# Kernel tuning notes

Hardware: AMD Instinct MI355X
Metric: run time of the kernel (lower is better)

The kernel has to match this reference:

```python
import jax, jax.numpy as jnp
import numpy as np

NUM_CLASSES = 20
MIN_CLASS_SIZE = 5000
EPS = 1e-6

B, C, H, W = 2, 64, 384, 384


def setup_inputs() -> dict:
    key = jax.random.key(0)
    k1, k2, k3 = jax.random.split(key, 3)
    hyperspectral_image = jax.random.normal(k1, (B, C, H, W), dtype=jnp.float32)
    methane_pattern = jax.random.normal(k2, (C,), dtype=jnp.float32)
    segmentation_mask = jax.random.randint(k3, (B, H, W), 0, NUM_CLASSES, dtype=jnp.int32)
    return {
        "hyperspectral_image": hyperspectral_image,
        "methane_pattern": methane_pattern,
        "segmentation_mask": segmentation_mask,
    }


def reference(hyperspectral_image, methane_pattern, segmentation_mask):
    b, c, h, w = hyperspectral_image.shape
    n = h * w
    # pixels: (B, N, C); seg: (B, N)
    x = jnp.transpose(hyperspectral_image, (0, 2, 3, 1)).reshape(b, n, c)
    seg = segmentation_mask.reshape(b, n)
    onehot = jax.nn.one_hot(seg, NUM_CLASSES, dtype=x.dtype)  # (B, N, K)

    counts = onehot.sum(axis=1)                                # (B, K)
    safe_counts = jnp.maximum(counts, 1.0)
    sums = jnp.einsum('bnk,bnc->bkc', onehot, x)               # (B, K, C)
    mean = sums / safe_counts[..., None]                       # (B, K, C)

    # Second moment per class: X_k^T X_k, then cov = E[xx^T] - mu mu^T + eps*I
    sxx = jnp.einsum('bnk,bnc,bnd->bkcd', onehot, x, x)        # (B, K, C, C)
    cov = sxx / safe_counts[..., None, None] - jnp.einsum('bkc,bkd->bkcd', mean, mean)
    cov = cov + EPS * jnp.eye(c, dtype=x.dtype)
    inv_cov = jnp.linalg.inv(cov)                              # (B, K, C, C)

    p = methane_pattern
    w_filt = jnp.einsum('bkcd,d->bkc', inv_cov, p)             # Sigma^-1 p, (B, K, C)
    denom = jnp.sqrt(jnp.einsum('c,bkc->bk', p, w_filt))       # (B, K)

    valid = (counts >= MIN_CLASS_SIZE).astype(x.dtype)         # (B, K)

    # Gather per-pixel class stats via one-hot (exact partition)
    mean_px = jnp.einsum('bnk,bkc->bnc', onehot, mean)         # (B, N, C)
    w_px = jnp.einsum('bnk,bkc->bnc', onehot, w_filt)          # (B, N, C)
    denom_px = jnp.einsum('bnk,bk->bn', onehot, denom)         # (B, N)
    valid_px = jnp.einsum('bnk,bk->bn', onehot, valid)         # (B, N)

    score = jnp.sum((x - mean_px) * w_px, axis=-1) / denom_px  # (B, N)
    score = score * valid_px
    return score.reshape(b, h, w)
```

## Files before the change

kernel.cpp:

```cpp
#include <hip/hip_runtime.h>
#include <math.h>

#define NCLS 20
#define CH 64
#define NPIX (384*384)
#define BATCH 2
#define MINSZ 5000
#define EPSV 1e-6f
#define NCHUNK 16
#define NBLK (BATCH*NPIX/256)
#define BLKPERB (NPIX/256)
#define PSTRIDE 4160
#define XSTR 72
#define ROWOFF(c) ((c)*XSTR + ((c)>>3)*8)

typedef __attribute__((ext_vector_type(8))) __bf16 bf16x8;
typedef __attribute__((ext_vector_type(4))) float  f32x4;

static __device__ inline unsigned short f2bf(float f) {
    unsigned u = __builtin_bit_cast(unsigned, f);
    return (unsigned short)((u + 0x7fffu + ((u >> 16) & 1u)) >> 16);
}
static __device__ inline float bf2f(unsigned us) {
    unsigned u = us << 16;
    return __builtin_bit_cast(float, u);
}

__global__ void k_hist(const int* __restrict__ seg, int* __restrict__ hist) {
    __shared__ int h[NCLS];
    int t = threadIdx.x;
    if (t < NCLS) h[t] = 0;
    __syncthreads();
    int k = seg[blockIdx.x * 256 + t];
    atomicAdd(&h[k], 1);
    __syncthreads();
    if (t < NCLS) hist[blockIdx.x * NCLS + t] = h[t];
}

__global__ void __launch_bounds__(256) k_scanall(const int* __restrict__ hist,
        int* __restrict__ counts, int* __restrict__ blockbase, int* __restrict__ offsets) {
    int bk = blockIdx.x;
    int b = bk / NCLS, k = bk % NCLS;
    int t = threadIdx.x;
    __shared__ int sh[BLKPERB];
    __shared__ int part[NCLS][12];
    __shared__ int ctot[NCLS];
    __shared__ int tpA[256], tpB[256];
    __shared__ int soff;

    const int* hb = hist + (size_t)b * BLKPERB * NCLS;
    for (int e = t; e < BLKPERB; e += 256) sh[e] = hb[e * NCLS + k];
    if (t < NCLS * 12) {
        int kk = t / 12, sub = t % 12;
        int s = 0;
        #pragma unroll 8
        for (int e = sub * 48; e < sub * 48 + 48; ++e) s += hb[e * NCLS + kk];
        part[kk][sub] = s;
    }
    __syncthreads();
    if (t < NCLS) {
        int s = 0;
        #pragma unroll
        for (int j = 0; j < 12; ++j) s += part[t][j];
        ctot[t] = s;
    }
    __syncthreads();
    if (t == 0) {
        int off = b * NPIX;
        for (int kk = 0; kk < k; ++kk) off += ctot[kk];
        soff = off;
        offsets[bk] = off;
        counts[bk] = ctot[k];
    }
    int s0 = 0, s1 = 0, s2 = 0;
    if (t < 192) {
        s0 = sh[3*t];
        s1 = s0 + sh[3*t + 1];
        s2 = s1 + sh[3*t + 2];
    }
    int mytot = (t < 192) ? s2 : 0;
    tpA[t] = mytot;
    __syncthreads();
    tpB[t] = tpA[t] + ((t >= 1)   ? tpA[t-1]   : 0); __syncthreads();
    tpA[t] = tpB[t] + ((t >= 2)   ? tpB[t-2]   : 0); __syncthreads();
    tpB[t] = tpA[t] + ((t >= 4)   ? tpA[t-4]   : 0); __syncthreads();
    tpA[t] = tpB[t] + ((t >= 8)   ? tpB[t-8]   : 0); __syncthreads();
    tpB[t] = tpA[t] + ((t >= 16)  ? tpA[t-16]  : 0); __syncthreads();
    tpA[t] = tpB[t] + ((t >= 32)  ? tpB[t-32]  : 0); __syncthreads();
    tpB[t] = tpA[t] + ((t >= 64)  ? tpA[t-64]  : 0); __syncthreads();
    tpA[t] = tpB[t] + ((t >= 128) ? tpB[t-128] : 0); __syncthreads();
    if (t < 192) {
        int excl = soff + tpA[t] - mytot;
        int* bb = blockbase + ((size_t)b * BLKPERB) * NCLS + k;
        bb[(3*t    ) * NCLS] = excl;
        bb[(3*t + 1) * NCLS] = excl + s0;
        bb[(3*t + 2) * NCLS] = excl + s1;
    }
}

__global__ void __launch_bounds__(256) k_scatter(const float* __restrict__ x, const int* __restrict__ seg,
                          const int* __restrict__ blockbase, unsigned short* __restrict__ gathered) {
    __shared__ float tile[256 * 33];
    __shared__ int wcnt[4][NCLS];
    __shared__ int sblk[NCLS];
    __shared__ int drow[256];
    int t = threadIdx.x;
    int blk = blockIdx.x;
    int base = blk * 256;
    int b = base / NPIX;
    int n = (base % NPIX) + t;
    int k = seg[base + t];
    int wave = t >> 6, lane = t & 63;

    int riw = 0;
    for (int cls = 0; cls < NCLS; ++cls) {
        unsigned long long m = __ballot(k == cls);
        if (lane == 0) wcnt[wave][cls] = __popcll(m);
        if (k == cls) riw = __popcll(m & ((1ull << lane) - 1ull));
    }
    __syncthreads();
    if (t < NCLS) {
        int s = 0;
        for (int c = 0; c < t; ++c) s += wcnt[0][c] + wcnt[1][c] + wcnt[2][c] + wcnt[3][c];
        sblk[t] = s;
    }
    __syncthreads();
    int rib = riw;
    for (int w = 0; w < 4; ++w) if (w < wave) rib += wcnt[w][k];
    int slot = sblk[k] + rib;
    drow[slot] = blockbase[blk * NCLS + k] + rib;
    const float* xb = x + (size_t)b * CH * NPIX + n;

    for (int ph = 0; ph < 2; ++ph) {
        __syncthreads();
        #pragma unroll 8
        for (int c = 0; c < 32; ++c)
            tile[slot * 33 + c] = xb[(size_t)(ph * 32 + c) * NPIX];
        __syncthreads();
        #pragma unroll 8
        for (int it = 0; it < 16; ++it) {
            int f = it * 256 + t;
            int r = f >> 4, c2 = f & 15;
            float a = tile[r * 33 + c2 * 2];
            float bq = tile[r * 33 + c2 * 2 + 1];
            unsigned pk = (unsigned)f2bf(a) | ((unsigned)f2bf(bq) << 16);
            *(unsigned*)(gathered + (size_t)drow[r] * CH + ph * 32 + c2 * 2) = pk;
        }
    }
}

__global__ void __launch_bounds__(256) k_gemm(const unsigned short* __restrict__ gathered,
        const int* __restrict__ counts, const int* __restrict__ offsets,
        float* __restrict__ partials) {
    __shared__ __align__(16) unsigned short xt[64 * XSTR + 7 * 8];
    __shared__ float wsum[4][CH];
    int id = blockIdx.x;
    int chunk = id % NCHUNK;
    int bk = id / NCHUNK;
    int cnt = counts[bk];
    int off = offsets[bk];
    int csz = (cnt + NCHUNK - 1) / NCHUNK;
    int p0 = chunk * csz;
    int pend = min(cnt, p0 + csz);
    int t = threadIdx.x;
    int w = t >> 6, l = t & 63, g = l >> 4, c15 = l & 15;
    int cg = t & 7;
    int ppair = t >> 3;

    f32x4 acc[4];
    #pragma unroll
    for (int nb = 0; nb < 4; ++nb) { f32x4 z = {0.f,0.f,0.f,0.f}; acc[nb] = z; }
    float ssum[8] = {0.f,0.f,0.f,0.f,0.f,0.f,0.f,0.f};

    for (int tp = p0; tp < pend; tp += 64) {
        __syncthreads();
        {
            int gp0 = tp + 2 * ppair, gp1 = gp0 + 1;
            uint4 v0 = make_uint4(0u,0u,0u,0u), v1 = make_uint4(0u,0u,0u,0u);
            if (gp0 < pend) v0 = *(const uint4*)(gathered + (size_t)(off + gp0) * CH + cg * 8);
            if (gp1 < pend) v1 = *(const uint4*)(gathered + (size_t)(off + gp1) * CH + cg * 8);
            unsigned a0[4] = {v0.x, v0.y, v0.z, v0.w};
            unsigned a1[4] = {v1.x, v1.y, v1.z, v1.w};
            #pragma unroll
            for (int q = 0; q < 4; ++q) {
                unsigned lo0 = a0[q] & 0xffffu, hi0 = a0[q] >> 16;
                unsigned lo1 = a1[q] & 0xffffu, hi1 = a1[q] >> 16;
                ssum[2*q]   += bf2f(lo0) + bf2f(lo1);
                ssum[2*q+1] += bf2f(hi0) + bf2f(hi1);
                int ch0 = 8 * cg + 2 * q;
                *(unsigned*)(xt + ROWOFF(ch0)     + 2 * ppair) = lo0 | (lo1 << 16);
                *(unsigned*)(xt + ROWOFF(ch0 + 1) + 2 * ppair) = hi0 | (hi1 << 16);
            }
        }
        __syncthreads();
        #pragma unroll
        for (int kc = 0; kc < 2; ++kc) {
            bf16x8 fr0 = *(const bf16x8*)(xt + ROWOFF( 0 + c15) + kc * 32 + 8 * g);
            bf16x8 fr1 = *(const bf16x8*)(xt + ROWOFF(16 + c15) + kc * 32 + 8 * g);
            bf16x8 fr2 = *(const bf16x8*)(xt + ROWOFF(32 + c15) + kc * 32 + 8 * g);
            bf16x8 fr3 = *(const bf16x8*)(xt + ROWOFF(48 + c15) + kc * 32 + 8 * g);
            bf16x8 fa;
            if      (w == 0) fa = fr0;
            else if (w == 1) fa = fr1;
            else if (w == 2) fa = fr2;
            else             fa = fr3;
            acc[0] = __builtin_amdgcn_mfma_f32_16x16x32_bf16(fa, fr0, acc[0], 0, 0, 0);
            acc[1] = __builtin_amdgcn_mfma_f32_16x16x32_bf16(fa, fr1, acc[1], 0, 0, 0);
            acc[2] = __builtin_amdgcn_mfma_f32_16x16x32_bf16(fa, fr2, acc[2], 0, 0, 0);
            acc[3] = __builtin_amdgcn_mfma_f32_16x16x32_bf16(fa, fr3, acc[3], 0, 0, 0);
        }
    }

    float* pout = partials + (size_t)id * PSTRIDE;
    #pragma unroll
    for (int nb = 0; nb < 4; ++nb)
        #pragma unroll
        for (int r = 0; r < 4; ++r)
            pout[(16*w + 4*g + r) * 64 + 16*nb + c15] = acc[nb][r];

    #pragma unroll
    for (int o = 8; o < 64; o <<= 1)
        #pragma unroll
        for (int j = 0; j < 8; ++j) ssum[j] += __shfl_xor(ssum[j], o);
    if (l < 8) {
        #pragma unroll
        for (int j = 0; j < 8; ++j) wsum[w][l * 8 + j] = ssum[j];
    }
    __syncthreads();
    if (t < CH) pout[4096 + t] = wsum[0][t] + wsum[1][t] + wsum[2][t] + wsum[3][t];
}

__global__ void __launch_bounds__(256) k_solve(const float* __restrict__ partials,
        const int* __restrict__ counts, const float* __restrict__ pattern,
        float* __restrict__ params) {
    int bk = blockIdx.x;
    int t = threadIdx.x;
    __shared__ float M[64][67];
    __shared__ float ssum[CH];
    __shared__ float wv[CH];
    __shared__ float red[2];

    const float* pp = partials + (size_t)bk * NCHUNK * PSTRIDE;
    int cnt = counts[bk];
    float inv = 1.0f / fmaxf((float)cnt, 1.0f);
    if (t < CH) {
        float v = 0.f;
        #pragma unroll
        for (int ch = 0; ch < NCHUNK; ++ch) v += pp[(size_t)ch * PSTRIDE + 4096 + t];
        ssum[t] = v;
    }
    __syncthreads();
    for (int e = t; e < 4096; e += 256) {
        float v = 0.f;
        #pragma unroll
        for (int ch = 0; ch < NCHUNK; ++ch) v += pp[(size_t)ch * PSTRIDE + e];
        int c = e >> 6, d = e & 63;
        float cov = v * inv - (ssum[c] * inv) * (ssum[d] * inv);
        if (c == d) cov += EPSV;
        M[c][d] = cov;
    }
    if (t < CH) M[t][64] = pattern[t];
    __syncthreads();

    int r = t >> 2, q = t & 3;
    for (int j = 0; j < 64; ++j) {
        float f = M[r][j] / M[j][j];
        if (r != j) {
            #pragma unroll 4
            for (int d = j + 1 + q; d <= 64; d += 4)
                M[r][d] -= f * M[j][d];
        }
        __syncthreads();
    }
    if (t < CH) wv[t] = M[t][64] / M[t][t];
    __syncthreads();

    if (t < CH) {
        float wvt = wv[t];
        float dp = pattern[t] * wvt;
        float bias = (ssum[t] * inv) * wvt;
        #pragma unroll
        for (int o = 32; o > 0; o >>= 1) {
            dp += __shfl_xor(dp, o);
            bias += __shfl_xor(bias, o);
        }
        if (t == 0) {
            float denom = sqrtf(dp);
            float valid = (cnt >= MINSZ) ? 1.0f : 0.0f;
            float scale = (denom > 0.f) ? (valid / denom) : 0.0f;
            red[0] = scale;
            red[1] = bias * scale;
        }
    }
    __syncthreads();
    if (t < CH) params[bk*66 + t] = wv[t] * red[0];
    if (t == 0) params[bk*66 + 64] = red[1];
    if (t == 1) params[bk*66 + 65] = 0.f;
}

__global__ void k_score(const float* __restrict__ x, const int* __restrict__ seg,
                        const float* __restrict__ params, float* __restrict__ out) {
    __shared__ float pw[NCLS][66];
    int t = threadIdx.x;
    int base = blockIdx.x * 256;
    int b = base / NPIX;
    for (int e = t; e < NCLS*66; e += 256)
        ((float*)pw)[e] = params[b*NCLS*66 + e];
    __syncthreads();

    int k = seg[base + t];
    int n = (base % NPIX) + t;
    const float* xb = x + (size_t)b * CH * NPIX + n;
    float a0 = 0.f, a1 = 0.f, a2 = 0.f, a3 = 0.f;
    #pragma unroll
    for (int c = 0; c < CH; c += 4) {
        a0 += xb[(size_t)(c+0) * NPIX] * pw[k][c+0];
        a1 += xb[(size_t)(c+1) * NPIX] * pw[k][c+1];
        a2 += xb[(size_t)(c+2) * NPIX] * pw[k][c+2];
        a3 += xb[(size_t)(c+3) * NPIX] * pw[k][c+3];
    }
    out[base + t] = (a0 + a1) + (a2 + a3) - pw[k][64];
}

extern "C" void kernel_launch(void* const* d_in, const int* in_sizes, int n_in,
                              void* d_out, int out_size, void* d_ws, size_t ws_size,
                              hipStream_t stream) {
    const float* x       = (const float*)d_in[0];
    const float* pattern = (const float*)d_in[1];
    const int*   seg     = (const int*)d_in[2];
    float* out = (float*)d_out;

    unsigned short* gathered = (unsigned short*)d_ws;
    float* partials = (float*)(gathered + (size_t)BATCH * NPIX * CH);
    float* params   = partials + (size_t)BATCH * NCLS * NCHUNK * PSTRIDE;
    int* hist      = (int*)(params + BATCH * NCLS * 66);
    int* blockbase = hist + NBLK * NCLS;
    int* counts    = blockbase + NBLK * NCLS;
    int* offsets   = counts + BATCH * NCLS;

    k_hist   <<<NBLK,               256, 0, stream>>>(seg, hist);
    k_scanall<<<BATCH*NCLS,         256, 0, stream>>>(hist, counts, blockbase, offsets);
    k_scatter<<<NBLK,               256, 0, stream>>>(x, seg, blockbase, gathered);
    k_gemm   <<<BATCH*NCLS*NCHUNK,  256, 0, stream>>>(gathered, counts, offsets, partials);
    k_solve  <<<BATCH*NCLS,         256, 0, stream>>>(partials, counts, pattern, params);
    k_score  <<<NBLK,               256, 0, stream>>>(x, seg, params, out);
}
```

Before: 105.8 us.

## Split partial reduction into its own kernel and solve with register-resident single-wave elimination

Moves the 16-chunk reduction of the second-moment partials out of k_solve into a new k_reduce kernel spread over 680 blocks, so the reduction is no longer serialized inside only 40 blocks. k_solve becomes a single 64-lane wavefront in which each lane holds one column of the covariance matrix in registers. It runs forward elimination with the pivot row broadcast through shared memory, then back-substitution, replacing the 256-thread Gauss-Jordan that synchronized every step. In exchange it adds a kernel launch and an extra global round trip, carries heavy register pressure from two 64-element per-lane arrays, and uses elimination without pivoting.

```diff
diff --git a/kernel.cpp b/kernel.cpp
--- a/kernel.cpp
+++ b/kernel.cpp
@@ -230,72 +230,124 @@
     if (t < CH) pout[4096 + t] = wsum[0][t] + wsum[1][t] + wsum[2][t] + wsum[3][t];
 }
 
-__global__ void __launch_bounds__(256) k_solve(const float* __restrict__ partials,
+__global__ void __launch_bounds__(256) k_reduce(const float* __restrict__ partials,
+        float* __restrict__ sxxred) {
+    int id = blockIdx.x;
+    int bk = id / 17, slice = id % 17;
+    int t = threadIdx.x;
+    const float* pp = partials + (size_t)bk * NCHUNK * PSTRIDE;
+    if (slice < 16) {
+        int e = slice * 256 + t;
+        float v = 0.f;
+        #pragma unroll
+        for (int ch = 0; ch < NCHUNK; ++ch) v += pp[(size_t)ch * PSTRIDE + e];
+        sxxred[(size_t)bk * PSTRIDE + e] = v;
+    } else if (t < CH) {
+        float v = 0.f;
+        #pragma unroll
+        for (int ch = 0; ch < NCHUNK; ++ch) v += pp[(size_t)ch * PSTRIDE + 4096 + t];
+        sxxred[(size_t)bk * PSTRIDE + 4096 + t] = v;
+    }
+}
+
+__global__ void __launch_bounds__(64) k_solve(const float* __restrict__ sxxred,
         const int* __restrict__ counts, const float* __restrict__ pattern,
         float* __restrict__ params) {
     int bk = blockIdx.x;
-    int t = threadIdx.x;
-    __shared__ float M[64][67];
-    __shared__ float ssum[CH];
-    __shared__ float wv[CH];
-    __shared__ float red[2];
-
-    const float* pp = partials + (size_t)bk * NCHUNK * PSTRIDE;
+    int lane = threadIdx.x;
+    __shared__ __align__(16) float srow[2][64];
+    __shared__ __align__(16) float sfb[2][64];
+    __shared__ float spinv[64];
+    __shared__ float ssm[64];
+    __shared__ float spat[64];
+
+    const float* pp = sxxred + (size_t)bk * PSTRIDE;
     int cnt = counts[bk];
     float inv = 1.0f / fmaxf((float)cnt, 1.0f);
-    if (t < CH) {
-        float v = 0.f;
-        #pragma unroll
-        for (int ch = 0; ch < NCHUNK; ++ch) v += pp[(size_t)ch * PSTRIDE + 4096 + t];
-        ssum[t] = v;
-    }
-    __syncthreads();
-    for (int e = t; e < 4096; e += 256) {
-        float v = 0.f;
-        #pragma unroll
-        for (int ch = 0; ch < NCHUNK; ++ch) v += pp[(size_t)ch * PSTRIDE + e];
-        int c = e >> 6, d = e & 63;
-        float cov = v * inv - (ssum[c] * inv) * (ssum[d] * inv);
-        if (c == d) cov += EPSV;
-        M[c][d] = cov;
-    }
-    if (t < CH) M[t][64] = pattern[t];
-    __syncthreads();
-
-    int r = t >> 2, q = t & 3;
+    ssm[lane] = pp[4096 + lane];
+    spat[lane] = pattern[lane];
+    __syncthreads();
+
+    float Mc[64];
+    float rhs[64];
+    float mean_d = ssm[lane] * inv;
+    #pragma unroll
+    for (int r = 0; r < 64; ++r) {
+        float s = pp[r * 64 + lane];
+        float cov = s * inv - (ssm[r] * inv) * mean_d;
+        Mc[r] = cov + ((r == lane) ? EPSV : 0.f);
+        rhs[r] = spat[r];
+    }
+
+    #pragma unroll
     for (int j = 0; j < 64; ++j) {
-        float f = M[r][j] / M[j][j];
-        if (r != j) {
-            #pragma unroll 4
-            for (int d = j + 1 + q; d <= 64; d += 4)
-                M[r][d] -= f * M[j][d];
-        }
-        __syncthreads();
-    }
-    if (t < CH) wv[t] = M[t][64] / M[t][t];
-    __syncthreads();
-
-    if (t < CH) {
-        float wvt = wv[t];
-        float dp = pattern[t] * wvt;
-        float bias = (ssum[t] * inv) * wvt;
-        #pragma unroll
-        for (int o = 32; o > 0; o >>= 1) {
-            dp += __shfl_xor(dp, o);
-            bias += __shfl_xor(bias, o);
-        }
-        if (t == 0) {
-            float denom = sqrtf(dp);
-            float valid = (cnt >= MINSZ) ? 1.0f : 0.0f;
-            float scale = (denom > 0.f) ? (valid / denom) : 0.0f;
-            red[0] = scale;
-            red[1] = bias * scale;
-        }
-    }
-    __syncthreads();
-    if (t < CH) params[bk*66 + t] = wv[t] * red[0];
-    if (t == 0) params[bk*66 + 64] = red[1];
-    if (t == 1) params[bk*66 + 65] = 0.f;
+        srow[j & 1][lane] = Mc[j];
+        __syncthreads();
+        float pinv = 1.0f / srow[j & 1][j];
+        if (lane == 0) spinv[j] = pinv;
+        #pragma unroll
+        for (int i = (j + 1) >> 2; i < 16; ++i) {
+            float4 rv = *((const float4*)srow[j & 1] + i);
+            float rvq[4] = {rv.x, rv.y, rv.z, rv.w};
+            #pragma unroll
+            for (int q = 0; q < 4; ++q) {
+                int r = 4 * i + q;
+                if (r > j) {
+                    float tf = rvq[q] * pinv;
+                    Mc[r]  = fmaf(-tf, Mc[j],  Mc[r]);
+                    rhs[r] = fmaf(-tf, rhs[j], rhs[r]);
+                }
+            }
+        }
+        __syncthreads();
+    }
+
+    #pragma unroll
+    for (int jj = 0; jj < 64; ++jj) {
+        int j = 63 - jj;
+        int nch = (j + 3) >> 2;
+        if (lane == j) {
+            #pragma unroll
+            for (int i = 0; i < 16; ++i) {
+                if (i < nch)
+                    *((float4*)sfb[jj & 1] + i) =
+                        make_float4(Mc[4*i], Mc[4*i+1], Mc[4*i+2], Mc[4*i+3]);
+            }
+        }
+        __syncthreads();
+        float tj = rhs[j] * spinv[j];
+        #pragma unroll
+        for (int i = 0; i < 16; ++i) {
+            if (i < nch) {
+                float4 rv = *((const float4*)sfb[jj & 1] + i);
+                float rvq[4] = {rv.x, rv.y, rv.z, rv.w};
+                #pragma unroll
+                for (int q = 0; q < 4; ++q) {
+                    int r = 4 * i + q;
+                    if (r < j) rhs[r] = fmaf(-rvq[q], tj, rhs[r]);
+                }
+            }
+        }
+    }
+
+    __syncthreads();
+    float dp = 0.f, bias = 0.f;
+    #pragma unroll
+    for (int r = 0; r < 64; ++r) {
+        float wr = rhs[r] * spinv[r];
+        dp   = fmaf(spat[r], wr, dp);
+        bias = fmaf(ssm[r] * inv, wr, bias);
+        rhs[r] = wr;
+    }
+    float denom = sqrtf(dp);
+    float valid = (cnt >= MINSZ) ? 1.0f : 0.0f;
+    float scale = (denom > 0.f) ? (valid / denom) : 0.0f;
+    if (lane == 0) {
+        #pragma unroll
+        for (int r = 0; r < 64; ++r) params[bk*66 + r] = rhs[r] * scale;
+        params[bk*66 + 64] = bias * scale;
+        params[bk*66 + 65] = 0.f;
+    }
 }
 
 __global__ void k_score(const float* __restrict__ x, const int* __restrict__ seg,
@@ -332,7 +384,8 @@
 
     unsigned short* gathered = (unsigned short*)d_ws;
     float* partials = (float*)(gathered + (size_t)BATCH * NPIX * CH);
-    float* params   = partials + (size_t)BATCH * NCLS * NCHUNK * PSTRIDE;
+    float* sxxred   = partials + (size_t)BATCH * NCLS * NCHUNK * PSTRIDE;
+    float* params   = sxxred + (size_t)BATCH * NCLS * PSTRIDE;
     int* hist      = (int*)(params + BATCH * NCLS * 66);
     int* blockbase = hist + NBLK * NCLS;
     int* counts    = blockbase + NBLK * NCLS;
@@ -342,6 +395,7 @@
     k_scanall<<<BATCH*NCLS,         256, 0, stream>>>(hist, counts, blockbase, offsets);
     k_scatter<<<NBLK,               256, 0, stream>>>(x, seg, blockbase, gathered);
     k_gemm   <<<BATCH*NCLS*NCHUNK,  256, 0, stream>>>(gathered, counts, offsets, partials);
-    k_solve  <<<BATCH*NCLS,         256, 0, stream>>>(partials, counts, pattern, params);
+    k_reduce <<<BATCH*NCLS*17,      256, 0, stream>>>(partials, sxxred);
+    k_solve  <<<BATCH*NCLS,          64, 0, stream>>>(sxxred, counts, pattern, params);
     k_score  <<<NBLK,               256, 0, stream>>>(x, seg, params, out);
 }
```

Result: slower. 156.9 us (+48.2%).
